# Performance work log

Measured on AMD Instinct MI355X. Metric: run time of the kernel, lower is better.

The kernel has to match this reference:

```python
import jax, jax.numpy as jnp
import numpy as np
from jax.scipy.special import logsumexp

SEQ, BATCH, NUM_TAGS = 1024, 512, 64


def setup_inputs() -> dict:
    key = jax.random.key(0)
    k_em, k_tag, k_len, k_s, k_e, k_t = jax.random.split(key, 6)
    emissions = jax.random.normal(k_em, (SEQ, BATCH, NUM_TAGS), dtype=jnp.float32)
    tags = jax.random.randint(k_tag, (SEQ, BATCH), 0, NUM_TAGS, dtype=jnp.int64)
    # random sequence lengths in [1, SEQ]; mask[0] is guaranteed all ones
    lengths = jax.random.randint(k_len, (BATCH,), 1, SEQ + 1)
    mask = (jnp.arange(SEQ)[:, None] < lengths[None, :]).astype(jnp.int32)
    # CRF params: uniform(-0.1, 0.1) as in reset_parameters()
    u = lambda k, shape: jax.random.uniform(k, shape, jnp.float32, -0.1, 0.1)
    return {
        "emissions": emissions,
        "tags": tags,
        "mask": mask,
        "start_transitions": u(k_s, (NUM_TAGS,)),
        "end_transitions": u(k_e, (NUM_TAGS,)),
        "transitions": u(k_t, (NUM_TAGS, NUM_TAGS)),
    }


def _compute_score(emissions, tags, maskf, start_transitions, end_transitions, transitions):
    # emissions: (S,B,T), tags/maskf: (S,B)
    S, B = tags.shape
    em_scores = jnp.take_along_axis(emissions, tags[:, :, None], axis=2)[..., 0]  # (S,B)
    trans_scores = transitions[tags[:-1], tags[1:]]  # (S-1,B)
    score = start_transitions[tags[0]] + em_scores[0]
    score = score + jnp.sum((trans_scores + em_scores[1:]) * maskf[1:], axis=0)
    seq_ends = maskf.astype(jnp.int32).sum(axis=0) - 1  # (B,)
    last_tags = tags[seq_ends, jnp.arange(B)]
    return score + end_transitions[last_tags]


def _compute_normalizer(emissions, mask, start_transitions, end_transitions, transitions):
    # forward algorithm: sequential logsumexp scan over timesteps
    def step(score, x):  # score: (B,T)
        em_t, m_t = x  # (B,T), (B,)
        nxt = logsumexp(score[:, :, None] + transitions[None, :, :] + em_t[:, None, :], axis=1)
        score = jnp.where(m_t[:, None] > 0, nxt, score)
        return score, None

    score0 = start_transitions[None, :] + emissions[0]  # (B,T)
    score, _ = jax.lax.scan(step, score0, (emissions[1:], mask[1:]))
    return logsumexp(score + end_transitions[None, :], axis=1)  # (B,)


def reference(emissions, tags, mask, start_transitions, end_transitions, transitions):
    maskf = mask.astype(emissions.dtype)
    numerator = _compute_score(emissions, tags, maskf, start_transitions, end_transitions, transitions)
    denominator = _compute_normalizer(emissions, mask, start_transitions, end_transitions, transitions)
    llh = numerator - denominator
    return llh.sum()  # reduction='sum' (default)
```

## Files before the change

### kernel.cpp

```cpp
#include <hip/hip_runtime.h>

#define SEQ 1024
#define BATCH 512
#define NTAGS 64
#define HALF_T 512
#define LOGD 4.158883083f

typedef _Float16 v2h __attribute__((ext_vector_type(2)));

#define FENCE() asm volatile("" ::: "memory")

__device__ __forceinline__ float dot2acc(v2h a, v2h b, float c) {
#if __has_builtin(__builtin_amdgcn_fdot2)
    return __builtin_amdgcn_fdot2(a, b, c, false);
#else
    return fmaf((float)a.x, (float)b.x, fmaf((float)a.y, (float)b.y, c));
#endif
}

__device__ __forceinline__ float rfl(float x) {
    return __uint_as_float(__builtin_amdgcn_readfirstlane(__float_as_uint(x)));
}

__global__ __launch_bounds__(64)
void scan_kernel(const float* __restrict__ em,
                 const int* __restrict__ mask,
                 const float* __restrict__ startT,
                 const float* __restrict__ endT,
                 const float* __restrict__ trans,
                 float* __restrict__ beta_f, float* __restrict__ Mf,
                 float* __restrict__ gma,    float* __restrict__ Mb,
                 int* __restrict__ Lw)
{
    const bool fwd = blockIdx.x < BATCH;
    const int  b   = fwd ? blockIdx.x : blockIdx.x - BATCH;
    const int  j   = threadIdx.x;

    __shared__ __align__(16) _Float16 bsh[NTAGS];

    int lsum = 0;
#pragma unroll
    for (int k = 0; k < SEQ / 64; ++k)
        lsum += mask[(k * 64 + j) * BATCH + b];
#pragma unroll
    for (int off = 32; off > 0; off >>= 1)
        lsum += __shfl_xor(lsum, off);
    const int L = lsum;

    v2h w[32];
#pragma unroll
    for (int i = 0; i < 32; ++i) {
        float a0, a1;
        if (fwd) { a0 = trans[(2 * i) * NTAGS + j]; a1 = trans[(2 * i + 1) * NTAGS + j]; }
        else     { a0 = trans[j * NTAGS + 2 * i];   a1 = trans[j * NTAGS + 2 * i + 1];   }
        v2h t; t.x = (_Float16)__expf(a0); t.y = (_Float16)__expf(a1);
        w[i] = t;
    }

    const float4* bv = (const float4*)bsh;

#define DOT(WRVAL, SOUT)                                                   \
    {                                                                      \
        FENCE();                                                           \
        bsh[j] = (_Float16)(WRVAL);                                        \
        FENCE();                                                           \
        float s0 = 0.f, s1 = 0.f, s2 = 0.f, s3 = 0.f;                      \
        _Pragma("unroll")                                                  \
        for (int q4 = 0; q4 < 8; ++q4) {                                   \
            float4 q = bv[q4];                                             \
            s0 = dot2acc(__builtin_bit_cast(v2h, q.x), w[4 * q4 + 0], s0); \
            s1 = dot2acc(__builtin_bit_cast(v2h, q.y), w[4 * q4 + 1], s1); \
            s2 = dot2acc(__builtin_bit_cast(v2h, q.z), w[4 * q4 + 2], s2); \
            s3 = dot2acc(__builtin_bit_cast(v2h, q.w), w[4 * q4 + 3], s3); \
        }                                                                  \
        SOUT = (s0 + s1) + (s2 + s3);                                      \
    }

    float beta, M;
    int nsteps = 0;

    if (fwd) {
        float em0 = em[(size_t)b * NTAGS + j];
        float a0  = startT[j] + em0;
        M    = __shfl(a0, 0);
        beta = __expf(a0 - M);

        const int Lf = min(L - 1, HALF_T - 1);
        int t = 1;
        float cur[4], nxt[4];
#pragma unroll
        for (int u = 0; u < 4; ++u) {
            cur[u] = em[((size_t)min(t + u,     SEQ - 1) * BATCH + b) * NTAGS + j];
            nxt[u] = em[((size_t)min(t + 4 + u, SEQ - 1) * BATCH + b) * NTAGS + j];
        }
        while (t + 3 <= Lf) {
            float pre[4];
#pragma unroll
            for (int u = 0; u < 4; ++u)
                pre[u] = em[((size_t)min(t + 8 + u, SEQ - 1) * BATCH + b) * NTAGS + j];
            float eem[4];
#pragma unroll
            for (int u = 0; u < 4; ++u) eem[u] = __expf(cur[u] - LOGD);

            float s;
            DOT(beta, s); beta = s * eem[0];
            DOT(beta, s);
            float r = rfl(s);
            beta = s * eem[1];
            DOT(beta, s); beta = s * eem[2];
            float rinv = 1.0f / r;
            float lr   = __logf(r);
            DOT(beta, s); beta = s * (eem[3] * rinv);
            M += lr;
            nsteps += 4;
#pragma unroll
            for (int u = 0; u < 4; ++u) { cur[u] = nxt[u]; nxt[u] = pre[u]; }
            t += 4;
        }
        for (; t <= Lf; ++t) {
            float emt = em[((size_t)t * BATCH + b) * NTAGS + j];
            float s; DOT(beta, s);
            beta = s * __expf(emt - LOGD);
            ++nsteps;
        }

        beta_f[b * NTAGS + j] = beta;
        if (j == 0) {
            Mf[b] = fmaf((float)nsteps, LOGD, M);
            Lw[b] = L;
        }
    } else {
        beta = __expf(endT[j]);
        M = 0.0f;
        if (L - 1 >= HALF_T) {
            int tt = L - 1;
            float cur[4], nxt[4];
#pragma unroll
            for (int u = 0; u < 4; ++u) {
                cur[u] = em[((size_t)max(tt - u,     0) * BATCH + b) * NTAGS + j];
                nxt[u] = em[((size_t)max(tt - 4 - u, 0) * BATCH + b) * NTAGS + j];
            }
            while (tt - 3 >= HALF_T) {
                float pre[4];
#pragma unroll
                for (int u = 0; u < 4; ++u)
                    pre[u] = em[((size_t)max(tt - 8 - u, 0) * BATCH + b) * NTAGS + j];
                float eem[4];
#pragma unroll
                for (int u = 0; u < 4; ++u) eem[u] = __expf(cur[u] - LOGD);

                float s;
                DOT(beta * eem[0], s); beta = s;
                DOT(beta * eem[1], s);
                float r = rfl(s);
                beta = s;
                DOT(beta * eem[2], s); beta = s;
                float rinv = 1.0f / r;
                float lr   = __logf(r);
                DOT(beta * (eem[3] * rinv), s); beta = s;
                M += lr;
                nsteps += 4;
#pragma unroll
                for (int u = 0; u < 4; ++u) { cur[u] = nxt[u]; nxt[u] = pre[u]; }
                tt -= 4;
            }
            for (; tt >= HALF_T; --tt) {
                float emt = em[((size_t)tt * BATCH + b) * NTAGS + j];
                float s; DOT(beta * __expf(emt - LOGD), s);
                beta = s;
                ++nsteps;
            }
        }
        gma[b * NTAGS + j] = beta;
        if (j == 0)
            Mb[b] = fmaf((float)nsteps, LOGD, M);
    }
#undef DOT
}

__global__ __launch_bounds__(64)
void join_kernel(const float* __restrict__ em,
                 const int* __restrict__ tags,
                 const float* __restrict__ startT,
                 const float* __restrict__ endT,
                 const float* __restrict__ trans,
                 const float* __restrict__ beta_f, const float* __restrict__ Mf,
                 const float* __restrict__ gma,    const float* __restrict__ Mb,
                 const int* __restrict__ Lw,
                 float* __restrict__ out)
{
    const int b = blockIdx.x;
    const int j = threadIdx.x;

    __shared__ float tr_sh[NTAGS * NTAGS];
#pragma unroll
    for (int i = 0; i < NTAGS; ++i)
        tr_sh[i * NTAGS + j] = trans[i * NTAGS + j];
    __syncthreads();

    const int L = Lw[b];

    float np = 0.0f;
#pragma unroll
    for (int k = 0; k < SEQ / 64; ++k) {
        int t = k * 64 + j;
        if (t >= 1 && t < L) {
            int ct = tags[t * BATCH + b];
            int pt = tags[(t - 1) * BATCH + b];
            np += tr_sh[pt * NTAGS + ct] + em[((size_t)t * BATCH + b) * NTAGS + ct];
        }
    }
    if (j == 0) {
        int t0 = tags[b];
        np += startT[t0] + em[(size_t)b * NTAGS + t0]
            + endT[tags[(size_t)(L - 1) * BATCH + b]];
    }

    float p = beta_f[b * NTAGS + j] * gma[b * NTAGS + j];

#pragma unroll
    for (int off = 32; off > 0; off >>= 1) {
        np += __shfl_xor(np, off);
        p  += __shfl_xor(p,  off);
    }

    if (j == 0) {
        float denom = __logf(p) + Mf[b] + Mb[b];
        atomicAdd(out, np - denom);
    }
}

extern "C" void kernel_launch(void* const* d_in, const int* in_sizes, int n_in,
                              void* d_out, int out_size, void* d_ws, size_t ws_size,
                              hipStream_t stream)
{
    const float* em     = (const float*)d_in[0];
    const int*   tags   = (const int*)d_in[1];
    const int*   mask   = (const int*)d_in[2];
    const float* startT = (const float*)d_in[3];
    const float* endT   = (const float*)d_in[4];
    const float* trans  = (const float*)d_in[5];
    float*       out    = (float*)d_out;

    float* beta_f = (float*)d_ws;
    float* Mf     = beta_f + BATCH * NTAGS;
    float* gma    = Mf + BATCH;
    float* Mb     = gma + BATCH * NTAGS;
    int*   Lw     = (int*)(Mb + BATCH);

    hipMemsetAsync(out, 0, sizeof(float) * out_size, stream);
    scan_kernel<<<2 * BATCH, 64, 0, stream>>>(em, mask, startT, endT, trans,
                                              beta_f, Mf, gma, Mb, Lw);
    join_kernel<<<BATCH, 64, 0, stream>>>(em, tags, startT, endT, trans,
                                          beta_f, Mf, gma, Mb, Lw, out);
}
```

Measured before the change: 276.4 us.

## Fuse numerator scoring into forward/backward scan and slim join kernel

```diff
diff --git a/kernel.cpp b/kernel.cpp
--- a/kernel.cpp
+++ b/kernel.cpp
@@ -24,19 +24,25 @@
 
 __global__ __launch_bounds__(64)
 void scan_kernel(const float* __restrict__ em,
+                 const int* __restrict__ tags,
                  const int* __restrict__ mask,
                  const float* __restrict__ startT,
                  const float* __restrict__ endT,
                  const float* __restrict__ trans,
                  float* __restrict__ beta_f, float* __restrict__ Mf,
                  float* __restrict__ gma,    float* __restrict__ Mb,
-                 int* __restrict__ Lw)
+                 float* __restrict__ out)
 {
     const bool fwd = blockIdx.x < BATCH;
     const int  b   = fwd ? blockIdx.x : blockIdx.x - BATCH;
     const int  j   = threadIdx.x;
 
     __shared__ __align__(16) _Float16 bsh[NTAGS];
+    __shared__ float tr_sh[NTAGS * NTAGS];
+
+#pragma unroll
+    for (int i = 0; i < NTAGS; ++i)
+        tr_sh[i * NTAGS + j] = trans[i * NTAGS + j];
 
     int lsum = 0;
 #pragma unroll
@@ -56,6 +62,7 @@
         v2h t; t.x = (_Float16)__expf(a0); t.y = (_Float16)__expf(a1);
         w[i] = t;
     }
+    FENCE();
 
     const float4* bv = (const float4*)bsh;
 
@@ -64,40 +71,57 @@
         FENCE();                                                           \
         bsh[j] = (_Float16)(WRVAL);                                        \
         FENCE();                                                           \
-        float s0 = 0.f, s1 = 0.f, s2 = 0.f, s3 = 0.f;                      \
+        float a0=0.f,a1=0.f,a2=0.f,a3=0.f,a4=0.f,a5=0.f,a6=0.f,a7=0.f;     \
         _Pragma("unroll")                                                  \
-        for (int q4 = 0; q4 < 8; ++q4) {                                   \
-            float4 q = bv[q4];                                             \
-            s0 = dot2acc(__builtin_bit_cast(v2h, q.x), w[4 * q4 + 0], s0); \
-            s1 = dot2acc(__builtin_bit_cast(v2h, q.y), w[4 * q4 + 1], s1); \
-            s2 = dot2acc(__builtin_bit_cast(v2h, q.z), w[4 * q4 + 2], s2); \
-            s3 = dot2acc(__builtin_bit_cast(v2h, q.w), w[4 * q4 + 3], s3); \
+        for (int q4 = 0; q4 < 8; q4 += 2) {                                \
+            float4 qa = bv[q4], qb = bv[q4 + 1];                           \
+            a0 = dot2acc(__builtin_bit_cast(v2h, qa.x), w[4 * q4 + 0], a0);\
+            a1 = dot2acc(__builtin_bit_cast(v2h, qa.y), w[4 * q4 + 1], a1);\
+            a2 = dot2acc(__builtin_bit_cast(v2h, qa.z), w[4 * q4 + 2], a2);\
+            a3 = dot2acc(__builtin_bit_cast(v2h, qa.w), w[4 * q4 + 3], a3);\
+            a4 = dot2acc(__builtin_bit_cast(v2h, qb.x), w[4 * q4 + 4], a4);\
+            a5 = dot2acc(__builtin_bit_cast(v2h, qb.y), w[4 * q4 + 5], a5);\
+            a6 = dot2acc(__builtin_bit_cast(v2h, qb.z), w[4 * q4 + 6], a6);\
+            a7 = dot2acc(__builtin_bit_cast(v2h, qb.w), w[4 * q4 + 7], a7);\
         }                                                                  \
-        SOUT = (s0 + s1) + (s2 + s3);                                      \
+        SOUT = ((a0 + a4) + (a1 + a5)) + ((a2 + a6) + (a3 + a7));          \
     }
 
-    float beta, M;
-    int nsteps = 0;
+    float num = 0.0f;
 
     if (fwd) {
         float em0 = em[(size_t)b * NTAGS + j];
         float a0  = startT[j] + em0;
-        M    = __shfl(a0, 0);
-        beta = __expf(a0 - M);
+        float M    = __shfl(a0, 0);
+        float beta = __expf(a0 - M);
+        int nsteps = 0;
+
+        int t0 = tags[b];
+        num = startT[t0] + __shfl(em0, t0);
+        if (L <= HALF_T)
+            num += endT[tags[(size_t)(L - 1) * BATCH + b]];
 
         const int Lf = min(L - 1, HALF_T - 1);
         int t = 1;
-        float cur[4], nxt[4];
+        float cur[4], nxt[4]; int tgc[4], tgn[4];
 #pragma unroll
         for (int u = 0; u < 4; ++u) {
-            cur[u] = em[((size_t)min(t + u,     SEQ - 1) * BATCH + b) * NTAGS + j];
-            nxt[u] = em[((size_t)min(t + 4 + u, SEQ - 1) * BATCH + b) * NTAGS + j];
-        }
+            int ta = min(t + u, SEQ - 1), tb = min(t + 4 + u, SEQ - 1);
+            cur[u] = em[((size_t)ta * BATCH + b) * NTAGS + j];
+            nxt[u] = em[((size_t)tb * BATCH + b) * NTAGS + j];
+            tgc[u] = tags[ta * BATCH + b];
+            tgn[u] = tags[tb * BATCH + b];
+        }
+        int prev = t0;
+
         while (t + 3 <= Lf) {
-            float pre[4];
-#pragma unroll
-            for (int u = 0; u < 4; ++u)
-                pre[u] = em[((size_t)min(t + 8 + u, SEQ - 1) * BATCH + b) * NTAGS + j];
+            float pre[4]; int tgp[4];
+#pragma unroll
+            for (int u = 0; u < 4; ++u) {
+                int tp = min(t + 8 + u, SEQ - 1);
+                pre[u] = em[((size_t)tp * BATCH + b) * NTAGS + j];
+                tgp[u] = tags[tp * BATCH + b];
+            }
             float eem[4];
 #pragma unroll
             for (int u = 0; u < 4; ++u) eem[u] = __expf(cur[u] - LOGD);
@@ -113,12 +137,25 @@
             DOT(beta, s); beta = s * (eem[3] * rinv);
             M += lr;
             nsteps += 4;
-#pragma unroll
-            for (int u = 0; u < 4; ++u) { cur[u] = nxt[u]; nxt[u] = pre[u]; }
+
+            num += tr_sh[prev   * NTAGS + tgc[0]] + __shfl(cur[0], tgc[0]);
+            num += tr_sh[tgc[0] * NTAGS + tgc[1]] + __shfl(cur[1], tgc[1]);
+            num += tr_sh[tgc[1] * NTAGS + tgc[2]] + __shfl(cur[2], tgc[2]);
+            num += tr_sh[tgc[2] * NTAGS + tgc[3]] + __shfl(cur[3], tgc[3]);
+            prev = tgc[3];
+
+#pragma unroll
+            for (int u = 0; u < 4; ++u) {
+                cur[u] = nxt[u]; nxt[u] = pre[u];
+                tgc[u] = tgn[u]; tgn[u] = tgp[u];
+            }
             t += 4;
         }
         for (; t <= Lf; ++t) {
             float emt = em[((size_t)t * BATCH + b) * NTAGS + j];
+            int   ct  = tags[t * BATCH + b];
+            num += tr_sh[prev * NTAGS + ct] + __shfl(emt, ct);
+            prev = ct;
             float s; DOT(beta, s);
             beta = s * __expf(emt - LOGD);
             ++nsteps;
@@ -127,24 +164,34 @@
         beta_f[b * NTAGS + j] = beta;
         if (j == 0) {
             Mf[b] = fmaf((float)nsteps, LOGD, M);
-            Lw[b] = L;
+            atomicAdd(out, num);
         }
     } else {
-        beta = __expf(endT[j]);
-        M = 0.0f;
+        float beta = __expf(endT[j]);
+        float M = 0.0f;
+        int nsteps = 0;
+
         if (L - 1 >= HALF_T) {
             int tt = L - 1;
-            float cur[4], nxt[4];
+            float cur[4], nxt[4]; int tgc[4], tgn[4];
 #pragma unroll
             for (int u = 0; u < 4; ++u) {
-                cur[u] = em[((size_t)max(tt - u,     0) * BATCH + b) * NTAGS + j];
-                nxt[u] = em[((size_t)max(tt - 4 - u, 0) * BATCH + b) * NTAGS + j];
-            }
+                int ta = max(tt - u, 0), tb = max(tt - 4 - u, 0);
+                cur[u] = em[((size_t)ta * BATCH + b) * NTAGS + j];
+                nxt[u] = em[((size_t)tb * BATCH + b) * NTAGS + j];
+                tgc[u] = tags[ta * BATCH + b];
+                tgn[u] = tags[tb * BATCH + b];
+            }
+            num = endT[tgc[0]];
+
             while (tt - 3 >= HALF_T) {
-                float pre[4];
-#pragma unroll
-                for (int u = 0; u < 4; ++u)
-                    pre[u] = em[((size_t)max(tt - 8 - u, 0) * BATCH + b) * NTAGS + j];
+                float pre[4]; int tgp[4];
+#pragma unroll
+                for (int u = 0; u < 4; ++u) {
+                    int tp = max(tt - 8 - u, 0);
+                    pre[u] = em[((size_t)tp * BATCH + b) * NTAGS + j];
+                    tgp[u] = tags[tp * BATCH + b];
+                }
                 float eem[4];
 #pragma unroll
                 for (int u = 0; u < 4; ++u) eem[u] = __expf(cur[u] - LOGD);
@@ -160,74 +207,51 @@
                 DOT(beta * (eem[3] * rinv), s); beta = s;
                 M += lr;
                 nsteps += 4;
-#pragma unroll
-                for (int u = 0; u < 4; ++u) { cur[u] = nxt[u]; nxt[u] = pre[u]; }
+
+                num += tr_sh[tgc[1] * NTAGS + tgc[0]] + __shfl(cur[0], tgc[0]);
+                num += tr_sh[tgc[2] * NTAGS + tgc[1]] + __shfl(cur[1], tgc[1]);
+                num += tr_sh[tgc[3] * NTAGS + tgc[2]] + __shfl(cur[2], tgc[2]);
+                num += tr_sh[tgn[0] * NTAGS + tgc[3]] + __shfl(cur[3], tgc[3]);
+
+#pragma unroll
+                for (int u = 0; u < 4; ++u) {
+                    cur[u] = nxt[u]; nxt[u] = pre[u];
+                    tgc[u] = tgn[u]; tgn[u] = tgp[u];
+                }
                 tt -= 4;
             }
             for (; tt >= HALF_T; --tt) {
                 float emt = em[((size_t)tt * BATCH + b) * NTAGS + j];
+                int   ct  = tags[tt * BATCH + b];
+                int   pt  = tags[(tt - 1) * BATCH + b];
+                num += tr_sh[pt * NTAGS + ct] + __shfl(emt, ct);
                 float s; DOT(beta * __expf(emt - LOGD), s);
                 beta = s;
                 ++nsteps;
             }
         }
         gma[b * NTAGS + j] = beta;
-        if (j == 0)
+        if (j == 0) {
             Mb[b] = fmaf((float)nsteps, LOGD, M);
+            atomicAdd(out, num);
+        }
     }
 #undef DOT
 }
 
 __global__ __launch_bounds__(64)
-void join_kernel(const float* __restrict__ em,
-                 const int* __restrict__ tags,
-                 const float* __restrict__ startT,
-                 const float* __restrict__ endT,
-                 const float* __restrict__ trans,
-                 const float* __restrict__ beta_f, const float* __restrict__ Mf,
+void join_kernel(const float* __restrict__ beta_f, const float* __restrict__ Mf,
                  const float* __restrict__ gma,    const float* __restrict__ Mb,
-                 const int* __restrict__ Lw,
                  float* __restrict__ out)
 {
     const int b = blockIdx.x;
     const int j = threadIdx.x;
-
-    __shared__ float tr_sh[NTAGS * NTAGS];
-#pragma unroll
-    for (int i = 0; i < NTAGS; ++i)
-        tr_sh[i * NTAGS + j] = trans[i * NTAGS + j];
-    __syncthreads();
-
-    const int L = Lw[b];
-
-    float np = 0.0f;
-#pragma unroll
-    for (int k = 0; k < SEQ / 64; ++k) {
-        int t = k * 64 + j;
-        if (t >= 1 && t < L) {
-            int ct = tags[t * BATCH + b];
-            int pt = tags[(t - 1) * BATCH + b];
-            np += tr_sh[pt * NTAGS + ct] + em[((size_t)t * BATCH + b) * NTAGS + ct];
-        }
-    }
-    if (j == 0) {
-        int t0 = tags[b];
-        np += startT[t0] + em[(size_t)b * NTAGS + t0]
-            + endT[tags[(size_t)(L - 1) * BATCH + b]];
-    }
-
     float p = beta_f[b * NTAGS + j] * gma[b * NTAGS + j];
-
-#pragma unroll
-    for (int off = 32; off > 0; off >>= 1) {
-        np += __shfl_xor(np, off);
-        p  += __shfl_xor(p,  off);
-    }
-
-    if (j == 0) {
-        float denom = __logf(p) + Mf[b] + Mb[b];
-        atomicAdd(out, np - denom);
-    }
+#pragma unroll
+    for (int off = 32; off > 0; off >>= 1)
+        p += __shfl_xor(p, off);
+    if (j == 0)
+        atomicAdd(out, -(__logf(p) + Mf[b] + Mb[b]));
 }
 
 extern "C" void kernel_launch(void* const* d_in, const int* in_sizes, int n_in,
@@ -246,11 +270,9 @@
     float* Mf     = beta_f + BATCH * NTAGS;
     float* gma    = Mf + BATCH;
     float* Mb     = gma + BATCH * NTAGS;
-    int*   Lw     = (int*)(Mb + BATCH);
 
     hipMemsetAsync(out, 0, sizeof(float) * out_size, stream);
-    scan_kernel<<<2 * BATCH, 64, 0, stream>>>(em, mask, startT, endT, trans,
-                                              beta_f, Mf, gma, Mb, Lw);
-    join_kernel<<<BATCH, 64, 0, stream>>>(em, tags, startT, endT, trans,
-                                          beta_f, Mf, gma, Mb, Lw, out);
-}
+    scan_kernel<<<2 * BATCH, 64, 0, stream>>>(em, tags, mask, startT, endT, trans,
+                                              beta_f, Mf, gma, Mb, out);
+    join_kernel<<<BATCH, 64, 0, stream>>>(beta_f, Mf, gma, Mb, out);
+}
```

Result: slower. 348.3 us (+26.0%).
